# Performance work log

Hardware: AMD Instinct MI355X
Metric: run time of the kernel (lower is better)

The kernel has to match this reference:

```python
import jax, jax.numpy as jnp
import numpy as np

B, T, C = 512, 256, 384
HEAD_SIZE = 64
SCALE = np.float32(1.0 / np.sqrt(HEAD_SIZE))


def setup_inputs() -> dict:
    key = jax.random.key(0)
    kx, kq, kk, kv = jax.random.split(key, 4)
    return {
        "x": jax.random.normal(kx, (B, T, C), dtype=jnp.float32),
        "Wq": jax.random.normal(kq, (C, HEAD_SIZE), dtype=jnp.float32) * (C ** -0.5),
        "Wk": jax.random.normal(kk, (C, HEAD_SIZE), dtype=jnp.float32) * (C ** -0.5),
        "Wv": jax.random.normal(kv, (C, HEAD_SIZE), dtype=jnp.float32) * (C ** -0.5),
    }


def reference(x, Wq, Wk, Wv):
    # projections: [B,T,C] @ [C,H] -> [B,T,H]
    q = x @ Wq
    k = x @ Wk
    v = x @ Wv
    # raw scores [B,T,T]
    scores = jnp.einsum("bth,bsh->bts", q, k)
    # causal mask then scale (source masks with -inf before dividing; -inf/8 == -inf)
    causal = jnp.tril(jnp.ones((x.shape[1], x.shape[1]), dtype=bool))
    scores = jnp.where(causal, scores, -jnp.inf) * SCALE
    w = jax.nn.softmax(scores, axis=-1)
    # dropout is identity in eval mode
    return jnp.einsum("bts,bsh->bth", w, v)
```

## Files before the change

kernel.cpp:

```cpp
#include <hip/hip_runtime.h>
#include <hip/hip_bf16.h>
#include <math.h>

#define NB 512
#define NT 256
#define NC 384
#define NH 64

typedef __bf16 bf16x8 __attribute__((ext_vector_type(8)));
typedef unsigned short u16x8 __attribute__((ext_vector_type(8)));
typedef unsigned int   u32x4 __attribute__((ext_vector_type(4)));
typedef float f32x4 __attribute__((ext_vector_type(4)));

__device__ __forceinline__ unsigned short f2bf(float f) {
    union { float f; unsigned u; } v; v.f = f;
    unsigned r = v.u + 0x7FFFu + ((v.u >> 16) & 1u);
    return (unsigned short)(r >> 16);
}

__device__ __forceinline__ unsigned pack2(float a, float b) {
    return (unsigned)f2bf(a) | ((unsigned)f2bf(b) << 16);
}

__device__ __forceinline__ f32x4 mfma16(bf16x8 a, bf16x8 b, f32x4 c) {
    return __builtin_amdgcn_mfma_f32_16x16x32_bf16(a, b, c, 0, 0, 0);
}

__global__ void prep_w(const float* __restrict__ Wq, const float* __restrict__ Wk,
                       const float* __restrict__ Wv, unsigned short* __restrict__ Wf) {
    const int e = blockIdx.x * 256 + threadIdx.x;
    const int j  = e & 7;
    const int l  = (e >> 3) & 63;
    const int fi = e >> 9;
    const int kk = fi % 12;
    const int n  = fi / 12;
    const int g = l >> 4, col = l & 15;
    const int c = kk * 32 + g * 8 + j;
    const int h = (n & 3) * 16 + col;
    const float* W = (n < 4) ? Wq : (n < 8 ? Wk : Wv);
    Wf[e] = f2bf(W[c * 64 + h]);
}

#define FOFF_Q   0
#define FLDQK    72
#define FOFF_K   18432
#define FOFF_VT  36864
#define FLDVT    264
#define FOFF_XS  53760
#define FLDXS    392
#define FSMEM    78848

__global__ __launch_bounds__(1024, 1) void head_v6(
    const float* __restrict__ x, const unsigned short* __restrict__ Wf,
    float* __restrict__ out)
{
    __shared__ __align__(16) unsigned short SM[FSMEM];

    const int b    = blockIdx.x;
    const int tid  = threadIdx.x;
    const int w    = tid >> 6;
    const int lane = tid & 63;
    const int g    = lane >> 4;
    const int col  = lane & 15;

    const int wq2 = w >> 2;
    const int T = (wq2 == 0) ? w : (wq2 == 1) ? (19 - w) : (wq2 == 2) ? (15 - w) : (w - 4);

    const int pass = w >> 2;
    const int n    = w & 3;
    bf16x8 Bw[12];
    if (w < 12) {
        #pragma unroll
        for (int kk = 0; kk < 12; ++kk)
            Bw[kk] = *reinterpret_cast<const bf16x8*>(
                Wf + ((size_t)((pass * 4 + n) * 12 + kk) * 64 + lane) * 8);
    }

    #pragma unroll 1
    for (int ch = 0; ch < 4; ++ch) {
        const float* xb = x + ((size_t)b * NT + ch * 64) * NC;
        #pragma unroll
        for (int k = 0; k < 3; ++k) {
            const int idx = k * 8192 + tid * 8;
            const int row = idx / 384;
            const int cc  = idx - row * 384;
            const float4 f0 = *reinterpret_cast<const float4*>(xb + idx);
            const float4 f1 = *reinterpret_cast<const float4*>(xb + idx + 4);
            u16x8 u;
            u[0] = f2bf(f0.x); u[1] = f2bf(f0.y); u[2] = f2bf(f0.z); u[3] = f2bf(f0.w);
            u[4] = f2bf(f1.x); u[5] = f2bf(f1.y); u[6] = f2bf(f1.z); u[7] = f2bf(f1.w);
            *reinterpret_cast<u16x8*>(&SM[FOFF_XS + row * FLDXS + cc]) = u;
        }
        __syncthreads();

        if (w < 12) {
            #pragma unroll
            for (int rt = 0; rt < 4; ++rt) {
                const int tile = ch * 4 + rt;
                f32x4 acc = (f32x4){0.f, 0.f, 0.f, 0.f};
                #pragma unroll
                for (int kk = 0; kk < 12; ++kk) {
                    const bf16x8 xf = *reinterpret_cast<const bf16x8*>(
                        &SM[FOFF_XS + (rt * 16 + col) * FLDXS + kk * 32 + g * 8]);
                    acc = mfma16(xf, Bw[kk], acc);
                }
                const int tb = tile * 16 + g * 4;
                if (pass < 2) {
                    const int base = (pass == 0) ? FOFF_Q : FOFF_K;
                    #pragma unroll
                    for (int r = 0; r < 4; ++r)
                        SM[base + (tb + r) * FLDQK + n * 16 + col] = f2bf(acc[r]);
                } else {
                    #pragma unroll
                    for (int r = 0; r < 4; ++r)
                        SM[FOFF_VT + (n * 16 + col) * FLDVT + tb + r] = f2bf(acc[r]);
                }
            }
        }
        __syncthreads();
    }

    const int hi_half = (lane >> 5) & 1;
    const int srcA = ((lane >> 4) & 1) * 32 + col;
    const int srcB = srcA + 16;

    bf16x8 qb[2];
    #pragma unroll
    for (int kk = 0; kk < 2; ++kk)
        qb[kk] = *reinterpret_cast<const bf16x8*>(
            &SM[FOFF_Q + (T * 16 + col) * FLDQK + kk * 32 + g * 8]);

    f32x4 sc[16];
    #pragma unroll
    for (int nt = 0; nt < 16; ++nt) {
        if (nt <= T) {
            f32x4 a = {0.f, 0.f, 0.f, 0.f};
            const bf16x8 ka0 = *reinterpret_cast<const bf16x8*>(
                &SM[FOFF_K + (nt * 16 + col) * FLDQK + g * 8]);
            const bf16x8 ka1 = *reinterpret_cast<const bf16x8*>(
                &SM[FOFF_K + (nt * 16 + col) * FLDQK + 32 + g * 8]);
            a = mfma16(ka0, qb[0], a);
            a = mfma16(ka1, qb[1], a);
            sc[nt] = a;
        }
    }

    float m = -INFINITY;
    #pragma unroll
    for (int nt = 0; nt < 16; ++nt) {
        if (nt <= T) {
            #pragma unroll
            for (int r = 0; r < 4; ++r) {
                float v = sc[nt][r] * 0.125f;
                if (nt == T && (4 * g + r) > col) v = -INFINITY;
                sc[nt][r] = v;
                m = fmaxf(m, v);
            }
        }
    }
    m = fmaxf(m, __shfl_xor(m, 16));
    m = fmaxf(m, __shfl_xor(m, 32));
    float s = 0.f;
    #pragma unroll
    for (int nt = 0; nt < 16; ++nt) {
        if (nt <= T) {
            #pragma unroll
            for (int r = 0; r < 4; ++r) {
                const float p = __expf(sc[nt][r] - m);
                sc[nt][r] = p;
                s += p;
            }
        }
    }
    s += __shfl_xor(s, 16);
    s += __shfl_xor(s, 32);
    const float inv = 1.0f / s;

    unsigned P4lo[16], P4hi[16];
    #pragma unroll
    for (int nt = 0; nt < 16; ++nt) {
        if (nt <= T) {
            P4lo[nt] = pack2(sc[nt][0] * inv, sc[nt][1] * inv);
            P4hi[nt] = pack2(sc[nt][2] * inv, sc[nt][3] * inv);
        } else { P4lo[nt] = 0u; P4hi[nt] = 0u; }
    }

    f32x4 oacc[4];
    #pragma unroll
    for (int nn = 0; nn < 4; ++nn) oacc[nn] = (f32x4){0.f, 0.f, 0.f, 0.f};
    #pragma unroll
    for (int cpv = 0; cpv < 8; ++cpv) {
        if (cpv <= (T >> 1)) {
            const unsigned a0 = __shfl(P4lo[2 * cpv],     srcA, 64);
            const unsigned a1 = __shfl(P4lo[2 * cpv + 1], srcA, 64);
            const unsigned b0 = __shfl(P4hi[2 * cpv],     srcA, 64);
            const unsigned b1 = __shfl(P4hi[2 * cpv + 1], srcA, 64);
            const unsigned c0 = __shfl(P4lo[2 * cpv],     srcB, 64);
            const unsigned c1 = __shfl(P4lo[2 * cpv + 1], srcB, 64);
            const unsigned d0 = __shfl(P4hi[2 * cpv],     srcB, 64);
            const unsigned d1 = __shfl(P4hi[2 * cpv + 1], srcB, 64);
            u32x4 wv;
            wv[0] = hi_half ? a1 : a0;
            wv[1] = hi_half ? b1 : b0;
            wv[2] = hi_half ? c1 : c0;
            wv[3] = hi_half ? d1 : d0;
            const bf16x8 pa = __builtin_bit_cast(bf16x8, wv);
            #pragma unroll
            for (int nn = 0; nn < 4; ++nn) {
                const bf16x8 vb = *reinterpret_cast<const bf16x8*>(
                    &SM[FOFF_VT + (nn * 16 + col) * FLDVT + cpv * 32 + g * 8]);
                oacc[nn] = mfma16(pa, vb, oacc[nn]);
            }
        }
    }

    #pragma unroll
    for (int nn = 0; nn < 4; ++nn)
        #pragma unroll
        for (int r = 0; r < 4; ++r)
            out[((size_t)b * NT + T * 16 + 4 * g + r) * NH + nn * 16 + col] = oacc[nn][r];
}

extern "C" void kernel_launch(void* const* d_in, const int* in_sizes, int n_in,
                              void* d_out, int out_size, void* d_ws, size_t ws_size,
                              hipStream_t stream) {
    (void)in_sizes; (void)n_in; (void)out_size; (void)ws_size;
    const float* x  = (const float*)d_in[0];
    const float* wq = (const float*)d_in[1];
    const float* wk = (const float*)d_in[2];
    const float* wv = (const float*)d_in[3];
    float* o = (float*)d_out;

    unsigned short* Wf = (unsigned short*)d_ws;
    prep_w <<<dim3(288), dim3(256),  0, stream>>>(wq, wk, wv, Wf);
    head_v6<<<dim3(NB),  dim3(1024), 0, stream>>>(x, Wf, o);
}
```

Baseline: 69.89 us.

## Double-buffer x chunks with register prefetch to overlap loads with projection MFMAs

```diff
diff --git a/kernel.cpp b/kernel.cpp
--- a/kernel.cpp
+++ b/kernel.cpp
@@ -9,6 +9,7 @@
 
 typedef __bf16 bf16x8 __attribute__((ext_vector_type(8)));
 typedef unsigned short u16x8 __attribute__((ext_vector_type(8)));
+typedef unsigned short u16x4 __attribute__((ext_vector_type(4)));
 typedef unsigned int   u32x4 __attribute__((ext_vector_type(4)));
 typedef float f32x4 __attribute__((ext_vector_type(4)));
 
@@ -46,11 +47,12 @@
 #define FOFF_K   18432
 #define FOFF_VT  36864
 #define FLDVT    264
-#define FOFF_XS  53760
+#define FOFF_XS0 53760
+#define FOFF_XS1 66304
 #define FLDXS    392
 #define FSMEM    78848
 
-__global__ __launch_bounds__(1024, 1) void head_v6(
+__global__ __launch_bounds__(1024, 1) void head_v7(
     const float* __restrict__ x, const unsigned short* __restrict__ Wf,
     float* __restrict__ out)
 {
@@ -76,32 +78,45 @@
                 Wf + ((size_t)((pass * 4 + n) * 12 + kk) * 64 + lane) * 8);
     }
 
+    const int srow[3] = { (tid * 4) / 384, (4096 + tid * 4) / 384, (8192 + tid * 4) / 384 };
+    const int scol[3] = { (tid * 4) % 384, (4096 + tid * 4) % 384, (8192 + tid * 4) % 384 };
+
+    {
+        const float* xb = x + (size_t)b * NT * NC;
+        float4 pre[3];
+        #pragma unroll
+        for (int k = 0; k < 3; ++k)
+            pre[k] = *reinterpret_cast<const float4*>(xb + k * 4096 + tid * 4);
+        #pragma unroll
+        for (int k = 0; k < 3; ++k) {
+            u16x4 u;
+            u[0] = f2bf(pre[k].x); u[1] = f2bf(pre[k].y);
+            u[2] = f2bf(pre[k].z); u[3] = f2bf(pre[k].w);
+            *reinterpret_cast<u16x4*>(&SM[FOFF_XS0 + srow[k] * FLDXS + scol[k]]) = u;
+        }
+    }
+    __syncthreads();
+
     #pragma unroll 1
-    for (int ch = 0; ch < 4; ++ch) {
-        const float* xb = x + ((size_t)b * NT + ch * 64) * NC;
-        #pragma unroll
-        for (int k = 0; k < 3; ++k) {
-            const int idx = k * 8192 + tid * 8;
-            const int row = idx / 384;
-            const int cc  = idx - row * 384;
-            const float4 f0 = *reinterpret_cast<const float4*>(xb + idx);
-            const float4 f1 = *reinterpret_cast<const float4*>(xb + idx + 4);
-            u16x8 u;
-            u[0] = f2bf(f0.x); u[1] = f2bf(f0.y); u[2] = f2bf(f0.z); u[3] = f2bf(f0.w);
-            u[4] = f2bf(f1.x); u[5] = f2bf(f1.y); u[6] = f2bf(f1.z); u[7] = f2bf(f1.w);
-            *reinterpret_cast<u16x8*>(&SM[FOFF_XS + row * FLDXS + cc]) = u;
-        }
-        __syncthreads();
-
+    for (int ch = 0; ch < 8; ++ch) {
+        float4 nxt[3];
+        if (ch < 7) {
+            const float* xb = x + ((size_t)b * NT + (ch + 1) * 32) * NC;
+            #pragma unroll
+            for (int k = 0; k < 3; ++k)
+                nxt[k] = *reinterpret_cast<const float4*>(xb + k * 4096 + tid * 4);
+        }
+
+        const int xsbase = (ch & 1) ? FOFF_XS1 : FOFF_XS0;
         if (w < 12) {
             #pragma unroll
-            for (int rt = 0; rt < 4; ++rt) {
-                const int tile = ch * 4 + rt;
+            for (int rt = 0; rt < 2; ++rt) {
+                const int tile = ch * 2 + rt;
                 f32x4 acc = (f32x4){0.f, 0.f, 0.f, 0.f};
                 #pragma unroll
                 for (int kk = 0; kk < 12; ++kk) {
                     const bf16x8 xf = *reinterpret_cast<const bf16x8*>(
-                        &SM[FOFF_XS + (rt * 16 + col) * FLDXS + kk * 32 + g * 8]);
+                        &SM[xsbase + (rt * 16 + col) * FLDXS + kk * 32 + g * 8]);
                     acc = mfma16(xf, Bw[kk], acc);
                 }
                 const int tb = tile * 16 + g * 4;
@@ -115,6 +130,18 @@
                     for (int r = 0; r < 4; ++r)
                         SM[FOFF_VT + (n * 16 + col) * FLDVT + tb + r] = f2bf(acc[r]);
                 }
+            }
+        }
+        __syncthreads();
+
+        if (ch < 7) {
+            const int nb = ((ch + 1) & 1) ? FOFF_XS1 : FOFF_XS0;
+            #pragma unroll
+            for (int k = 0; k < 3; ++k) {
+                u16x4 u;
+                u[0] = f2bf(nxt[k].x); u[1] = f2bf(nxt[k].y);
+                u[2] = f2bf(nxt[k].z); u[3] = f2bf(nxt[k].w);
+                *reinterpret_cast<u16x4*>(&SM[nb + srow[k] * FLDXS + scol[k]]) = u;
             }
         }
         __syncthreads();
@@ -233,5 +260,5 @@
 
     unsigned short* Wf = (unsigned short*)d_ws;
     prep_w <<<dim3(288), dim3(256),  0, stream>>>(wq, wk, wv, Wf);
-    head_v6<<<dim3(NB),  dim3(1024), 0, stream>>>(x, Wf, o);
-}
+    head_v7<<<dim3(NB),  dim3(1024), 0, stream>>>(x, Wf, o);
+}
```

Measured after the change: 58.17 us. -16.8%, faster.
